# Performance work log

Hardware: AMD Instinct MI355X
Metric: run time of the kernel (lower is better)

Reference implementation:

```python
import jax, jax.numpy as jnp
import numpy as np

N_VARS = 1024      # code length n
N_CHECKS = 512     # number of parity checks m
VAR_DEG = 3        # column degree -> E = N_VARS * VAR_DEG edges
N_EDGES = N_VARS * VAR_DEG
BATCH = 2048
CLIP_TANH = 10.0
ENSEMBLE_NUM = 3


def _make_edges():
    # Regular LDPC-like Tanner graph: each variable node connects to VAR_DEG distinct checks.
    rng = np.random.default_rng(0)
    edge_var = np.repeat(np.arange(N_VARS, dtype=np.int32), VAR_DEG)
    edge_chk = np.concatenate([
        rng.choice(N_CHECKS, size=VAR_DEG, replace=False).astype(np.int32)
        for _ in range(N_VARS)
    ])
    return jnp.asarray(edge_var), jnp.asarray(edge_chk)


def setup_inputs() -> dict:
    key = jax.random.key(0)
    k1, k2, k3, k4, k5 = jax.random.split(key, 5)
    edge_var, edge_chk = _make_edges()
    return {
        "x": jax.random.normal(k1, (BATCH, N_EDGES), dtype=jnp.float32),
        "llr": jax.random.normal(k2, (BATCH, N_VARS), dtype=jnp.float32),
        "odd_weights": jax.random.normal(k3, (N_EDGES, N_EDGES), dtype=jnp.float32) * 0.05,
        "llr_weights": jax.random.normal(k4, (N_VARS, N_EDGES), dtype=jnp.float32) * 0.05,
        "dropout_logits": jnp.full((N_EDGES,), 3.0, dtype=jnp.float32),  # LOGITS_INIT
        "edge_var": edge_var,
        "edge_chk": edge_chk,
    }


def reference(x, llr, odd_weights, llr_weights, dropout_logits, edge_var, edge_chk):
    dt = x.dtype
    # Tanner-graph masks (constant connectivity)
    # w_skipconn2even_mask: [n, E], 1 where edge e is incident to variable v
    w_skip_mask = (jnp.arange(N_VARS)[:, None] == edge_var[None, :]).astype(dt)
    # w_odd2even_mask: [E, E], 1 where edges share a variable but differ in check (extrinsic)
    w_odd_mask = ((edge_var[:, None] == edge_var[None, :]) &
                  (edge_chk[:, None] != edge_chk[None, :])).astype(dt)

    x_after_mask = x @ (w_odd_mask * odd_weights)                 # [B, E]
    odd_weights_times_llr = llr @ (w_skip_mask * llr_weights)     # [B, E]

    keep_prob = jax.nn.sigmoid(dropout_logits)                    # [E]
    keys = jax.random.split(jax.random.key(42), ENSEMBLE_NUM)

    def member(k):
        u = jax.random.uniform(k, odd_weights_times_llr.shape, dtype=dt)
        z = (u < keep_prob).astype(dt)                            # dropout_ori
        odd = jnp.clip(x_after_mask + odd_weights_times_llr * z,
                       -CLIP_TANH, CLIP_TANH)
        return jnp.tanh(0.5 * odd)

    return jnp.mean(jax.vmap(member)(keys), axis=0)              # ensemble average
```

## Files before the change

kernel.cpp:

```cpp
#include <hip/hip_runtime.h>
#include <stdint.h>
#include <cmath>

#define NVARS   1024
#define NEDGES  3072
#define BATCHSZ 2048
#define RPT     4
#define ROWSTR  (BATCHSZ/RPT)

__host__ __device__ __forceinline__ uint32_t rotl32(uint32_t x, int r) {
#if defined(__HIP_DEVICE_COMPILE__)
    return __builtin_amdgcn_alignbit(x, x, (uint32_t)(32 - r));
#else
    return (x << r) | (x >> (32 - r));
#endif
}

__host__ __forceinline__ void threefry2x32_host(uint32_t k0, uint32_t k1,
                                                uint32_t x0, uint32_t x1,
                                                uint32_t& o0, uint32_t& o1) {
    uint32_t k2 = k0 ^ k1 ^ 0x1BD11BDAu;
    const int rots[20] = {13,15,26,6, 17,29,16,24, 13,15,26,6, 17,29,16,24, 13,15,26,6};
    x0 += k0; x1 += k1;
    int rc = 0;
    const uint32_t ka[5] = {k1, k2, k0, k1, k2};
    const uint32_t kb[5] = {k2, k0, k1, k2, k0};
    for (int g = 0; g < 5; g++) {
        for (int i = 0; i < 4; i++) {
            x0 += x1; x1 = rotl32(x1, rots[rc++]); x1 ^= x0;
        }
        x0 += ka[g]; x1 += kb[g] + (uint32_t)(g + 1);
    }
    o0 = x0; o1 = x1;
}

__device__ __forceinline__ void threefry_quad_xor(
        uint32_t k0, uint32_t k1,
        uint32_t i0, uint32_t i1, uint32_t i2, uint32_t i3,
        uint32_t& m0, uint32_t& m1, uint32_t& m2, uint32_t& m3) {
    uint32_t k2 = k0 ^ k1 ^ 0x1BD11BDAu;
    uint32_t a0 = k0, a1 = i0 + k1;
    uint32_t b0 = k0, b1 = i1 + k1;
    uint32_t c0 = k0, c1 = i2 + k1;
    uint32_t d0 = k0, d1 = i3 + k1;
#define R4(r) \
    a0 += a1; b0 += b1; c0 += c1; d0 += d1; \
    a1 = rotl32(a1, r); b1 = rotl32(b1, r); c1 = rotl32(c1, r); d1 = rotl32(d1, r); \
    a1 ^= a0; b1 ^= b0; c1 ^= c0; d1 ^= d0;
#define INJ4(ka, kb) \
    a0 += (ka); b0 += (ka); c0 += (ka); d0 += (ka); \
    a1 += (kb); b1 += (kb); c1 += (kb); d1 += (kb);
    R4(13) R4(15) R4(26) R4(6)  INJ4(k1, k2 + 1u)
    R4(17) R4(29) R4(16) R4(24) INJ4(k2, k0 + 2u)
    R4(13) R4(15) R4(26) R4(6)  INJ4(k0, k1 + 3u)
    R4(17) R4(29) R4(16) R4(24) INJ4(k1, k2 + 4u)
    R4(13) R4(15) R4(26) R4(6)  INJ4(k2, k0 + 5u)
#undef R4
#undef INJ4
    m0 = a0 ^ a1; m1 = b0 ^ b1; m2 = c0 ^ c1; m3 = d0 ^ d1;
}

__device__ __forceinline__ float tanh_half(float o) {
    float ex = __expf(o);
    return 1.0f - 2.0f * __builtin_amdgcn_rcpf(ex + 1.0f);
}

__global__ void setup_kernel(const float* __restrict__ oddw,
                             const float* __restrict__ llrw,
                             const float* __restrict__ logits,
                             const int* __restrict__ evar,
                             const int* __restrict__ echk,
                             float4* __restrict__ wkp,
                             int4* __restrict__ sidx) {
    int e = blockIdx.x * blockDim.x + threadIdx.x;
    if (e >= NEDGES) return;
    int v = evar[e];
    int r = e % 3;
    int base = e - r;
    int o1 = base + ((r + 1) % 3);
    int o2 = base + ((r + 2) % 3);
    int ce = echk[e];
    float w1 = (echk[o1] != ce) ? oddw[(size_t)o1 * NEDGES + e] : 0.0f;
    float w2 = (echk[o2] != ce) ? oddw[(size_t)o2 * NEDGES + e] : 0.0f;
    float vw = llrw[(size_t)v * NEDGES + e];
    float kpf = (float)(1.0 / (1.0 + exp(-(double)logits[e])));
    double Td = ceil((double)kpf * 8388608.0);
    uint32_t T9;
    if (Td >= 8388608.0) T9 = 0xFFFFFFFFu;
    else                 T9 = ((uint32_t)Td) << 9;
    wkp[e]  = make_float4(w1, w2, vw, __uint_as_float(T9));
    sidx[e] = make_int4(o1, o2, v, 0);
}

#define ISTEP ((uint32_t)ROWSTR * NEDGES)
#define XSTEP (ISTEP * 4u)
#define LSTEP ((uint32_t)ROWSTR * NVARS * 4u)

__global__ __launch_bounds__(256, 8) void
odd_layer_kernel(const float* __restrict__ x, const float* __restrict__ llr,
                 const float4* __restrict__ wkp, const int4* __restrict__ sidx,
                 float* __restrict__ out,
                 uint32_t k0a, uint32_t k1a, uint32_t k0b, uint32_t k1b,
                 uint32_t k0c, uint32_t k1c) {
    const int e  = blockIdx.x * 256 + threadIdx.x;
    const int b0 = blockIdx.y;

    const char* xb = (const char*)(x   + (size_t)b0 * NEDGES);
    const char* lb = (const char*)(llr + (size_t)b0 * NVARS);
    char*       ob = (char*)      (out + (size_t)b0 * NEDGES);

    float4 w = wkp[e];
    int4   s = sidx[e];
    const uint32_t T9 = __float_as_uint(w.w);

    const uint32_t i0 = (uint32_t)b0 * NEDGES + (uint32_t)e;
    const uint32_t i1 = i0 + ISTEP, i2 = i0 + 2u * ISTEP, i3 = i0 + 3u * ISTEP;

    uint32_t p0, p1, p2, p3;
    threefry_quad_xor(k0a, k1a, i0, i1, i2, i3, p0, p1, p2, p3);

    const uint32_t sx4 = (uint32_t)s.x << 2;
    const uint32_t sy4 = (uint32_t)s.y << 2;
    const uint32_t sz4 = (uint32_t)s.z << 2;
    float xv1[RPT], xv2[RPT], lvv[RPT];
#pragma unroll
    for (int r = 0; r < RPT; r++) {
        xv1[r] = *(const float*)(xb + (sx4 + r * XSTEP));
        xv2[r] = *(const float*)(xb + (sy4 + r * XSTEP));
        lvv[r] = *(const float*)(lb + (sz4 + r * LSTEP));
    }

    uint32_t q0, q1, q2, q3, r0, r1, r2, r3;
    threefry_quad_xor(k0b, k1b, i0, i1, i2, i3, q0, q1, q2, q3);
    threefry_quad_xor(k0c, k1c, i0, i1, i2, i3, r0, r1, r2, r3);

    int cnt[RPT];
    cnt[0] = ((p0 < T9) ? 1 : 0) + ((q0 < T9) ? 1 : 0) + ((r0 < T9) ? 1 : 0);
    cnt[1] = ((p1 < T9) ? 1 : 0) + ((q1 < T9) ? 1 : 0) + ((r1 < T9) ? 1 : 0);
    cnt[2] = ((p2 < T9) ? 1 : 0) + ((q2 < T9) ? 1 : 0) + ((r2 < T9) ? 1 : 0);
    cnt[3] = ((p3 < T9) ? 1 : 0) + ((q3 < T9) ? 1 : 0) + ((r3 < T9) ? 1 : 0);

    const uint32_t e4 = (uint32_t)e << 2;
#pragma unroll
    for (int r = 0; r < RPT; r++) {
        float xa = fmaf(xv2[r], w.y, xv1[r] * w.x);
        float t0 = tanh_half(xa);
        float t1 = tanh_half(fmaf(lvv[r], w.z, xa));
        float cf = (float)cnt[r];
        *(float*)(ob + (e4 + r * XSTEP)) = fmaf(cf, (t1 - t0) * (1.0f / 3.0f), t0);
    }
}

extern "C" void kernel_launch(void* const* d_in, const int* in_sizes, int n_in,
                              void* d_out, int out_size, void* d_ws, size_t ws_size,
                              hipStream_t stream) {
    const float* x      = (const float*)d_in[0];
    const float* llr    = (const float*)d_in[1];
    const float* oddw   = (const float*)d_in[2];
    const float* llrw   = (const float*)d_in[3];
    const float* logits = (const float*)d_in[4];
    const int*   evar   = (const int*)d_in[5];
    const int*   echk   = (const int*)d_in[6];
    float* out = (float*)d_out;

    float4* wkp  = (float4*)d_ws;
    int4*   sidx = (int4*)((char*)d_ws + (size_t)NEDGES * sizeof(float4));

    uint32_t k0[3], k1[3];
    for (uint32_t j = 0; j < 3; j++) {
        threefry2x32_host(0u, 42u, 0u, j, k0[j], k1[j]);
    }

    setup_kernel<<<(NEDGES + 255) / 256, 256, 0, stream>>>(oddw, llrw, logits, evar, echk, wkp, sidx);

    dim3 grid(NEDGES / 256, ROWSTR);
    odd_layer_kernel<<<grid, 256, 0, stream>>>(x, llr, wkp, sidx, out,
                                               k0[0], k1[0], k0[1], k1[1], k0[2], k1[2]);
}
```

Baseline: 44.73 us.

## Flatten grid so each block handles three edge chunks with nontemporal stores

The 2D grid of 12x512 blocks becomes a 1D grid of 2048 blocks. Each block loops over three 256-edge chunks for one batch row-group, which cuts block count and amortises the per-block address setup. Output writes use nontemporal stores to avoid polluting the cache, and the setup kernel launches with 64-thread blocks. Fewer blocks may reduce latency hiding per CU, and the decode of blockIdx assumes ROWSTR is 512.

Measured after the change: 45.27 us. About the same (+1.2%).

```diff
diff --git a/kernel.cpp b/kernel.cpp
--- a/kernel.cpp
+++ b/kernel.cpp
@@ -7,6 +7,8 @@
 #define BATCHSZ 2048
 #define RPT     4
 #define ROWSTR  (BATCHSZ/RPT)
+#define NTILES  (12 * ROWSTR)
+#define GRID    2048
 
 __host__ __device__ __forceinline__ uint32_t rotl32(uint32_t x, int r) {
 #if defined(__HIP_DEVICE_COMPILE__)
@@ -102,52 +104,61 @@
                  float* __restrict__ out,
                  uint32_t k0a, uint32_t k1a, uint32_t k0b, uint32_t k1b,
                  uint32_t k0c, uint32_t k1c) {
-    const int e  = blockIdx.x * 256 + threadIdx.x;
-    const int b0 = blockIdx.y;
+    const int tid = threadIdx.x;
+    const int blk = blockIdx.x;
+    const int b0  = blk & (ROWSTR - 1);
+    const int ec0 = blk >> 9;
 
     const char* xb = (const char*)(x   + (size_t)b0 * NEDGES);
     const char* lb = (const char*)(llr + (size_t)b0 * NVARS);
     char*       ob = (char*)      (out + (size_t)b0 * NEDGES);
+    const uint32_t ibase = (uint32_t)b0 * NEDGES;
 
-    float4 w = wkp[e];
-    int4   s = sidx[e];
-    const uint32_t T9 = __float_as_uint(w.w);
+#pragma unroll
+    for (int it = 0; it < 3; ++it) {
+        const int e = (ec0 + it * 4) * 256 + tid;
 
-    const uint32_t i0 = (uint32_t)b0 * NEDGES + (uint32_t)e;
-    const uint32_t i1 = i0 + ISTEP, i2 = i0 + 2u * ISTEP, i3 = i0 + 3u * ISTEP;
+        float4 w = wkp[e];
+        int4   s = sidx[e];
+        const uint32_t T9 = __float_as_uint(w.w);
 
-    uint32_t p0, p1, p2, p3;
-    threefry_quad_xor(k0a, k1a, i0, i1, i2, i3, p0, p1, p2, p3);
+        const uint32_t i0 = ibase + (uint32_t)e;
+        const uint32_t i1 = i0 + ISTEP, i2 = i0 + 2u * ISTEP, i3 = i0 + 3u * ISTEP;
 
-    const uint32_t sx4 = (uint32_t)s.x << 2;
-    const uint32_t sy4 = (uint32_t)s.y << 2;
-    const uint32_t sz4 = (uint32_t)s.z << 2;
-    float xv1[RPT], xv2[RPT], lvv[RPT];
+        uint32_t p0, p1, p2, p3;
+        threefry_quad_xor(k0a, k1a, i0, i1, i2, i3, p0, p1, p2, p3);
+
+        const uint32_t sx4 = (uint32_t)s.x << 2;
+        const uint32_t sy4 = (uint32_t)s.y << 2;
+        const uint32_t sz4 = (uint32_t)s.z << 2;
+        float xv1[RPT], xv2[RPT], lvv[RPT];
 #pragma unroll
-    for (int r = 0; r < RPT; r++) {
-        xv1[r] = *(const float*)(xb + (sx4 + r * XSTEP));
-        xv2[r] = *(const float*)(xb + (sy4 + r * XSTEP));
-        lvv[r] = *(const float*)(lb + (sz4 + r * LSTEP));
-    }
+        for (int r = 0; r < RPT; r++) {
+            xv1[r] = *(const float*)(xb + (sx4 + r * XSTEP));
+            xv2[r] = *(const float*)(xb + (sy4 + r * XSTEP));
+            lvv[r] = *(const float*)(lb + (sz4 + r * LSTEP));
+        }
 
-    uint32_t q0, q1, q2, q3, r0, r1, r2, r3;
-    threefry_quad_xor(k0b, k1b, i0, i1, i2, i3, q0, q1, q2, q3);
-    threefry_quad_xor(k0c, k1c, i0, i1, i2, i3, r0, r1, r2, r3);
+        uint32_t q0, q1, q2, q3, r0, r1, r2, r3;
+        threefry_quad_xor(k0b, k1b, i0, i1, i2, i3, q0, q1, q2, q3);
+        threefry_quad_xor(k0c, k1c, i0, i1, i2, i3, r0, r1, r2, r3);
 
-    int cnt[RPT];
-    cnt[0] = ((p0 < T9) ? 1 : 0) + ((q0 < T9) ? 1 : 0) + ((r0 < T9) ? 1 : 0);
-    cnt[1] = ((p1 < T9) ? 1 : 0) + ((q1 < T9) ? 1 : 0) + ((r1 < T9) ? 1 : 0);
-    cnt[2] = ((p2 < T9) ? 1 : 0) + ((q2 < T9) ? 1 : 0) + ((r2 < T9) ? 1 : 0);
-    cnt[3] = ((p3 < T9) ? 1 : 0) + ((q3 < T9) ? 1 : 0) + ((r3 < T9) ? 1 : 0);
+        int cnt0 = ((p0 < T9) ? 1 : 0) + ((q0 < T9) ? 1 : 0) + ((r0 < T9) ? 1 : 0);
+        int cnt1 = ((p1 < T9) ? 1 : 0) + ((q1 < T9) ? 1 : 0) + ((r1 < T9) ? 1 : 0);
+        int cnt2 = ((p2 < T9) ? 1 : 0) + ((q2 < T9) ? 1 : 0) + ((r2 < T9) ? 1 : 0);
+        int cnt3 = ((p3 < T9) ? 1 : 0) + ((q3 < T9) ? 1 : 0) + ((r3 < T9) ? 1 : 0);
+        int cnt[RPT] = {cnt0, cnt1, cnt2, cnt3};
 
-    const uint32_t e4 = (uint32_t)e << 2;
+        const uint32_t e4 = (uint32_t)e << 2;
 #pragma unroll
-    for (int r = 0; r < RPT; r++) {
-        float xa = fmaf(xv2[r], w.y, xv1[r] * w.x);
-        float t0 = tanh_half(xa);
-        float t1 = tanh_half(fmaf(lvv[r], w.z, xa));
-        float cf = (float)cnt[r];
-        *(float*)(ob + (e4 + r * XSTEP)) = fmaf(cf, (t1 - t0) * (1.0f / 3.0f), t0);
+        for (int r = 0; r < RPT; r++) {
+            float xa = fmaf(xv2[r], w.y, xv1[r] * w.x);
+            float t0 = tanh_half(xa);
+            float t1 = tanh_half(fmaf(lvv[r], w.z, xa));
+            float cf = (float)cnt[r];
+            float res = fmaf(cf, (t1 - t0) * (1.0f / 3.0f), t0);
+            __builtin_nontemporal_store(res, (float*)(ob + (e4 + r * XSTEP)));
+        }
     }
 }
 
@@ -171,9 +182,8 @@
         threefry2x32_host(0u, 42u, 0u, j, k0[j], k1[j]);
     }
 
-    setup_kernel<<<(NEDGES + 255) / 256, 256, 0, stream>>>(oddw, llrw, logits, evar, echk, wkp, sidx);
+    setup_kernel<<<48, 64, 0, stream>>>(oddw, llrw, logits, evar, echk, wkp, sidx);
 
-    dim3 grid(NEDGES / 256, ROWSTR);
-    odd_layer_kernel<<<grid, 256, 0, stream>>>(x, llr, wkp, sidx, out,
+    odd_layer_kernel<<<GRID, 256, 0, stream>>>(x, llr, wkp, sidx, out,
                                                k0[0], k1[0], k0[1], k1[1], k0[2], k1[2]);
 }
```
